# Optimization experiments

Hardware: AMD Instinct MI355X
Metric: run time of the kernel (lower is better)

## Reference

```python
import jax, jax.numpy as jnp
import numpy as np

N, E, G = 10000, 160000, 64
NODE_DIM, HID = 128, 256


def _edge_conv(x, src, dst, w1, b1, w2, b2):
    # gather endpoints: x_i = target features, x_j = source features (PyG source_to_target)
    x_i = x[dst]                              # [E, C]
    x_j = x[src]                              # [E, C]
    m = jnp.concatenate([x_i, x_j - x_i], axis=-1)  # [E, 2C]
    m = jax.nn.relu(m @ w1 + b1) @ w2 + b2          # [E, H]
    out = jax.ops.segment_max(m, dst, num_segments=N)  # scatter-max per target node
    return out  # nodes with no in-edges get -inf; subsequent relu maps them to 0 (matches PyG fill 0 + relu)


def setup_inputs() -> dict:
    key = jax.random.key(0)
    ks = jax.random.split(key, 20)
    x = jax.random.normal(ks[0], (N, NODE_DIM), dtype=jnp.float32)
    edge_index = jax.random.randint(ks[1], (2, E), 0, N)
    batch = jnp.sort(jax.random.randint(ks[2], (N,), 0, G))
    s = 0.05
    inp = {"x": x, "edge_index": edge_index, "batch": batch}
    dims = [(2 * NODE_DIM, HID), (2 * HID, HID), (2 * HID, HID)]
    for li, (din, dout) in enumerate(dims):
        inp[f"c{li}_w1"] = jax.random.normal(ks[3 + 4 * li], (din, dout), jnp.float32) * s
        inp[f"c{li}_b1"] = jnp.zeros((dout,), jnp.float32)
        inp[f"c{li}_w2"] = jax.random.normal(ks[4 + 4 * li], (dout, dout), jnp.float32) * s
        inp[f"c{li}_b2"] = jnp.zeros((dout,), jnp.float32)
    inp["cl_w1"] = jax.random.normal(ks[15], (2 * HID, HID), jnp.float32) * s
    inp["cl_b1"] = jnp.zeros((HID,), jnp.float32)
    inp["cl_w2"] = jax.random.normal(ks[16], (HID, 64), jnp.float32) * s
    inp["cl_b2"] = jnp.zeros((64,), jnp.float32)
    inp["cl_w3"] = jax.random.normal(ks[17], (64, 1), jnp.float32) * s
    inp["cl_b3"] = jnp.zeros((1,), jnp.float32)
    return inp


def reference(x, edge_index, batch,
              c0_w1, c0_b1, c0_w2, c0_b2,
              c1_w1, c1_b1, c1_w2, c1_b2,
              c2_w1, c2_b1, c2_w2, c2_b2,
              cl_w1, cl_b1, cl_w2, cl_b2, cl_w3, cl_b3):
    src, dst = edge_index[0], edge_index[1]
    for (w1, b1, w2, b2) in [(c0_w1, c0_b1, c0_w2, c0_b2),
                             (c1_w1, c1_b1, c1_w2, c1_b2),
                             (c2_w1, c2_b1, c2_w2, c2_b2)]:
        x = jax.nn.relu(_edge_conv(x, src, dst, w1, b1, w2, b2))
    # global mean / max pool per graph
    sums = jax.ops.segment_sum(x, batch, num_segments=G)
    counts = jax.ops.segment_sum(jnp.ones((x.shape[0], 1), x.dtype), batch, num_segments=G)
    x_mean = sums / jnp.maximum(counts, 1.0)
    x_max = jax.ops.segment_max(x, batch, num_segments=G)
    x_max = jnp.where(counts > 0, x_max, 0.0)
    h = jnp.concatenate([x_mean, x_max], axis=1)  # [G, 2H]
    h = jax.nn.relu(h @ cl_w1 + cl_b1)            # dropout is eval-mode identity
    h = jax.nn.relu(h @ cl_w2 + cl_b2)
    out = (h @ cl_w3 + cl_b3).squeeze(-1)         # [G]
    return out
```

## Files before the change

### kernel.cpp

```cpp
#include <hip/hip_runtime.h>


#define NN 10000
#define NE 160000
#define NG 64
#define NP 10048
#define EB 64

typedef __attribute__((ext_vector_type(8))) _Float16 f16x8;
typedef __attribute__((ext_vector_type(4))) _Float16 f16x4;
typedef __attribute__((ext_vector_type(4))) float f32x4;

__global__ void hist_kernel(const int* __restrict__ dstI, int* __restrict__ hist) {
    int i = blockIdx.x * blockDim.x + threadIdx.x;
    if (i < NE) atomicAdd(&hist[dstI[i]], 1);
}

__global__ void scan_kernel(const int* __restrict__ hist, int* __restrict__ cursor) {
    __shared__ int sums[256];
    const int t = threadIdx.x;
    const int per = (NN + 255) / 256;
    const int lo = t * per, hi = (lo + per < NN) ? lo + per : NN;
    int s = 0;
    for (int i = lo; i < hi; ++i) s += hist[i];
    sums[t] = s;
    __syncthreads();
    for (int ofs = 1; ofs < 256; ofs <<= 1) {
        int add = (t >= ofs) ? sums[t - ofs] : 0;
        __syncthreads();
        sums[t] += add;
        __syncthreads();
    }
    int run = sums[t] - s;
    for (int i = lo; i < hi; ++i) {
        int h = hist[i];
        cursor[i] = run;
        run += h;
    }
}

__global__ void scatter_kernel(const int* __restrict__ srcI, const int* __restrict__ dstI,
                               int* __restrict__ cursor,
                               int* __restrict__ se2, int* __restrict__ de2) {
    int i = blockIdx.x * blockDim.x + threadIdx.x;
    if (i < NE) {
        int d = dstI[i];
        int p = atomicAdd(&cursor[d], 1);
        se2[p] = srcI[i];
        de2[p] = d;
    }
}

__global__ void prep_weights(const float* __restrict__ w1, const float* __restrict__ w2, int C,
                             _Float16* __restrict__ WcT, _Float16* __restrict__ w2T) {
    int total1 = 512 * C;
    int total = total1 + 256 * 256;
    for (int i = blockIdx.x * blockDim.x + threadIdx.x; i < total; i += gridDim.x * blockDim.x) {
        if (i < total1) {
            int n = i / C, k = i - n * C;
            float v = (n < 256) ? (w1[k * 256 + n] - w1[(C + k) * 256 + n])
                                : w1[(C + k) * 256 + (n - 256)];
            WcT[n * C + k] = (_Float16)v;
        } else {
            int j = i - total1;
            int n = j >> 8, k = j & 255;
            w2T[n * 256 + k] = (_Float16)w2[k * 256 + n];
        }
    }
}

template <int C>
__global__ void conv_rows(const float* __restrict__ src, _Float16* __restrict__ xh) {
    const int total4 = NP * C / 4;
    const int c4 = C / 4;
    for (int i4 = blockIdx.x * blockDim.x + threadIdx.x; i4 < total4; i4 += gridDim.x * blockDim.x) {
        const int row = i4 / c4;
        f16x4 o;
        if (row < NN) {
            float4 v = ((const float4*)src)[i4];
            o[0] = (_Float16)v.x; o[1] = (_Float16)v.y;
            o[2] = (_Float16)v.z; o[3] = (_Float16)v.w;
        } else {
            o[0] = o[1] = o[2] = o[3] = (_Float16)0.f;
        }
        ((f16x4*)xh)[i4] = o;
    }
}

template <int C>
__global__ __launch_bounds__(256) void node_gemm(
    const _Float16* __restrict__ xh, const _Float16* __restrict__ WT,
    const float* __restrict__ b1, float* __restrict__ Af, _Float16* __restrict__ Bh) {
    const int wave = threadIdx.x >> 6, lane = threadIdx.x & 63;
    const int lrow = lane & 15, lk = (lane >> 4) * 8;
    const int r0 = blockIdx.x * 64;
    const int c0 = blockIdx.y * 256 + wave * 64;

    f32x4 acc[4][4] = {};
#pragma unroll
    for (int kk = 0; kk < C; kk += 32) {
        f16x8 ah[4];
#pragma unroll
        for (int m = 0; m < 4; ++m)
            ah[m] = *(const f16x8*)(xh + (size_t)(r0 + m * 16 + lrow) * C + kk + lk);
#pragma unroll
        for (int t = 0; t < 4; ++t) {
            f16x8 bh = *(const f16x8*)(WT + (size_t)(c0 + t * 16 + lrow) * C + kk + lk);
#pragma unroll
            for (int m = 0; m < 4; ++m)
                acc[m][t] = __builtin_amdgcn_mfma_f32_16x16x32_f16(ah[m], bh, acc[m][t], 0, 0, 0);
        }
    }
    if (blockIdx.y == 0) {
#pragma unroll
        for (int t = 0; t < 4; ++t) {
            const int col = c0 + t * 16 + lrow;
            const float bias = b1[col];
#pragma unroll
            for (int m = 0; m < 4; ++m)
#pragma unroll
                for (int j = 0; j < 4; ++j) {
                    const int row = r0 + m * 16 + (lane >> 4) * 4 + j;
                    Af[(size_t)row * 256 + col] = acc[m][t][j] + bias;
                }
        }
    } else {
#pragma unroll
        for (int t = 0; t < 4; ++t) {
            const int col = c0 - 256 + t * 16 + lrow;
#pragma unroll
            for (int m = 0; m < 4; ++m)
#pragma unroll
                for (int j = 0; j < 4; ++j) {
                    const int row = r0 + m * 16 + (lane >> 4) * 4 + j;
                    Bh[(size_t)row * 256 + col] = (_Float16)acc[m][t][j];
                }
        }
    }
}

__global__ __launch_bounds__(512, 4) void edge_gemm(
    const float* __restrict__ Af, const _Float16* __restrict__ Bh,
    const int* __restrict__ se2, const int* __restrict__ de2,
    const _Float16* __restrict__ w2T,
    const float* __restrict__ b2, float* __restrict__ y) {
    __shared__ _Float16 hh[EB * 256];
    const int tid = threadIdx.x;
    const int wave = tid >> 6, lane = tid & 63;

    const int orig = blockIdx.x;
    const int xcd = orig & 7, pos = orig >> 3;
    const int q = 2500 >> 3, r = 2500 & 7;
    const int bid = (xcd < r ? xcd * (q + 1) : r * (q + 1) + (xcd - r) * q) + pos;
    const int e0 = bid * EB;

    {
        int se[8], de[8];
#pragma unroll
        for (int i = 0; i < 8; ++i) {
            se[i] = se2[e0 + wave * 8 + i];
            de[i] = de2[e0 + wave * 8 + i];
        }
        float4 av[8];
        f16x4 bv[8];
#pragma unroll
        for (int i = 0; i < 8; ++i) {
            bv[i] = *(const f16x4*)(Bh + (size_t)se[i] * 256 + lane * 4);
            av[i] = *(const float4*)(Af + (size_t)de[i] * 256 + lane * 4);
        }
#pragma unroll
        for (int i = 0; i < 8; ++i) {
            const int el = wave * 8 + i;
            const int row = ((el >> 2) & 3) * 16 + (el >> 4) * 4 + (el & 3);
            f16x4 vh;
            vh[0] = (_Float16)fmaxf(av[i].x + (float)bv[i][0], 0.f);
            vh[1] = (_Float16)fmaxf(av[i].y + (float)bv[i][1], 0.f);
            vh[2] = (_Float16)fmaxf(av[i].z + (float)bv[i][2], 0.f);
            vh[3] = (_Float16)fmaxf(av[i].w + (float)bv[i][3], 0.f);
            const int idx = (row * 256 + lane * 4) ^ ((row & 7) << 3);
            *(f16x4*)(&hh[idx]) = vh;
        }
    }
    __syncthreads();

    const int lrow = lane & 15, lk = (lane >> 4) * 8;
    const _Float16* wbase = w2T + (size_t)(wave * 32 + lrow) * 256 + lk;

    f32x4 acc[4][2] = {};
    f16x8 bhA[2], bhB[2];
    bhA[0] = *(const f16x8*)(wbase);
    bhA[1] = *(const f16x8*)(wbase + 16 * 256);
#pragma unroll
    for (int kk = 0; kk < 256; kk += 32) {
        if (kk + 32 < 256) {
            bhB[0] = *(const f16x8*)(wbase + kk + 32);
            bhB[1] = *(const f16x8*)(wbase + 16 * 256 + kk + 32);
        }
        f16x8 ah[4];
#pragma unroll
        for (int m = 0; m < 4; ++m) {
            const int row = m * 16 + lrow;
            const int idx = (row * 256 + kk + lk) ^ ((row & 7) << 3);
            ah[m] = *(const f16x8*)(&hh[idx]);
        }
#pragma unroll
        for (int t = 0; t < 2; ++t)
#pragma unroll
            for (int m = 0; m < 4; ++m)
                acc[m][t] = __builtin_amdgcn_mfma_f32_16x16x32_f16(ah[m], bhA[t], acc[m][t], 0, 0, 0);
        bhA[0] = bhB[0];
        bhA[1] = bhB[1];
    }

    const int g = lane >> 4;
    int d[16];
#pragma unroll
    for (int k = 0; k < 16; ++k) d[k] = de2[e0 + g * 16 + k];
#pragma unroll
    for (int t = 0; t < 2; ++t) {
        const int col = wave * 32 + t * 16 + lrow;
        const float bias = b2[col];
        float run = acc[0][t][0];
        int dp = d[0];
#pragma unroll
        for (int k = 1; k < 16; ++k) {
            const float v = acc[k >> 2][t][k & 3];
            if (d[k] == dp) {
                run = fmaxf(run, v);
            } else {
                const float o = run + bias;
                if (o > 0.f) atomicMax((int*)(y + (size_t)dp * 256 + col), __float_as_int(o));
                run = v;
                dp = d[k];
            }
        }
        const float o = run + bias;
        if (o > 0.f) atomicMax((int*)(y + (size_t)dp * 256 + col), __float_as_int(o));
    }
}

__global__ void pool_kernel(const float* __restrict__ y, const int* __restrict__ batch,
                            float* __restrict__ pooled) {
    const int g = blockIdx.x;
    __shared__ int slo, shi;
    if (threadIdx.x == 0) {
        int lo = 0, hi = NN;
        while (lo < hi) { int m = (lo + hi) >> 1; if (batch[m] < g) lo = m + 1; else hi = m; }
        slo = lo;
        int lo2 = lo, hi2 = NN;
        while (lo2 < hi2) { int m = (lo2 + hi2) >> 1; if (batch[m] < g + 1) lo2 = m + 1; else hi2 = m; }
        shi = lo2;
    }
    __syncthreads();
    const int lo = slo, hi = shi, c = threadIdx.x;
    float s0 = 0.f, s1 = 0.f, s2 = 0.f, s3 = 0.f;
    float m0 = 0.f, m1 = 0.f, m2 = 0.f, m3 = 0.f;
    int n = lo;
    for (; n + 4 <= hi; n += 4) {
        float v0 = y[(size_t)(n + 0) * 256 + c];
        float v1 = y[(size_t)(n + 1) * 256 + c];
        float v2 = y[(size_t)(n + 2) * 256 + c];
        float v3 = y[(size_t)(n + 3) * 256 + c];
        s0 += v0; s1 += v1; s2 += v2; s3 += v3;
        m0 = fmaxf(m0, v0); m1 = fmaxf(m1, v1); m2 = fmaxf(m2, v2); m3 = fmaxf(m3, v3);
    }
    for (; n < hi; ++n) {
        float v = y[(size_t)n * 256 + c];
        s0 += v; m0 = fmaxf(m0, v);
    }
    const float s = (s0 + s1) + (s2 + s3);
    const float mx = fmaxf(fmaxf(m0, m1), fmaxf(m2, m3));
    const int cnt = hi - lo;
    pooled[g * 512 + c] = cnt ? s / (float)cnt : 0.f;
    pooled[g * 512 + 256 + c] = cnt ? mx : 0.f;
}

__global__ void classifier(const float* __restrict__ pooled,
                           const float* __restrict__ w1, const float* __restrict__ b1,
                           const float* __restrict__ w2, const float* __restrict__ b2,
                           const float* __restrict__ w3, const float* __restrict__ b3,
                           float* __restrict__ out) {
    const int g = blockIdx.x;
    __shared__ float ph[512];
    __shared__ float o1[256];
    __shared__ float o2[64];
    const int t = threadIdx.x;
    ph[t] = pooled[g * 512 + t];
    ph[t + 256] = pooled[g * 512 + 256 + t];
    __syncthreads();
    float s = 0.f;
    for (int k = 0; k < 512; ++k) s += ph[k] * w1[k * 256 + t];
    o1[t] = fmaxf(s + b1[t], 0.f);
    __syncthreads();
    if (t < 64) {
        float s2 = 0.f;
        for (int k = 0; k < 256; ++k) s2 += o1[k] * w2[k * 64 + t];
        o2[t] = fmaxf(s2 + b2[t], 0.f);
    }
    __syncthreads();
    if (t < 64) {
        float v = o2[t] * w3[t];
        for (int off = 32; off; off >>= 1) v += __shfl_down(v, off);
        if (t == 0) out[g] = v + b3[0];
    }
}

extern "C" void kernel_launch(void* const* d_in, const int* in_sizes, int n_in,
                              void* d_out, int out_size, void* d_ws, size_t ws_size,
                              hipStream_t stream) {
    (void)in_sizes; (void)n_in; (void)out_size; (void)ws_size;
    const float* x0 = (const float*)d_in[0];
    const int* eidx = (const int*)d_in[1];
    const int* batch = (const int*)d_in[2];
    const int* srcI = eidx;
    const int* dstI = eidx + NE;

    char* ws = (char*)d_ws;
    size_t off = 0;
    auto alloc = [&](size_t bytes) -> void* {
        void* p = ws + off;
        off += (bytes + 255) & ~(size_t)255;
        return p;
    };
    _Float16* xh = (_Float16*)alloc((size_t)NP * 256 * 2);
    float* Af = (float*)alloc((size_t)NP * 256 * 4);
    _Float16* Bh = (_Float16*)alloc((size_t)NP * 256 * 2);
    float* y  = (float*)alloc((size_t)NP * 256 * 4);
    _Float16* WcT = (_Float16*)alloc(512 * 256 * 2);
    _Float16* w2T = (_Float16*)alloc(256 * 256 * 2);
    float* pooled = (float*)alloc(64 * 512 * 4);
    int* hist = (int*)alloc(NN * 4);
    int* se2 = (int*)alloc(NE * 4);
    int* de2 = (int*)alloc(NE * 4);

    const float* lw[3][4] = {
        {(const float*)d_in[3],  (const float*)d_in[4],  (const float*)d_in[5],  (const float*)d_in[6]},
        {(const float*)d_in[7],  (const float*)d_in[8],  (const float*)d_in[9],  (const float*)d_in[10]},
        {(const float*)d_in[11], (const float*)d_in[12], (const float*)d_in[13], (const float*)d_in[14]},
    };

    hipMemsetAsync(hist, 0, NN * 4, stream);
    hist_kernel<<<dim3((NE + 255) / 256), dim3(256), 0, stream>>>(dstI, hist);
    scan_kernel<<<dim3(1), dim3(256), 0, stream>>>(hist, hist);
    scatter_kernel<<<dim3((NE + 255) / 256), dim3(256), 0, stream>>>(srcI, dstI, hist, se2, de2);

    conv_rows<128><<<dim3(1024), dim3(256), 0, stream>>>(x0, xh);

    for (int l = 0; l < 3; ++l) {
        const int C = (l == 0) ? 128 : 256;
        prep_weights<<<dim3(256), dim3(256), 0, stream>>>(lw[l][0], lw[l][2], C, WcT, w2T);
        if (C == 128)
            node_gemm<128><<<dim3(NP / 64, 2), dim3(256), 0, stream>>>(xh, WcT, lw[l][1], Af, Bh);
        else
            node_gemm<256><<<dim3(NP / 64, 2), dim3(256), 0, stream>>>(xh, WcT, lw[l][1], Af, Bh);
        hipMemsetAsync(y, 0, (size_t)NP * 256 * 4, stream);
        edge_gemm<<<dim3(NE / EB), dim3(512), 0, stream>>>(Af, Bh, se2, de2, w2T, lw[l][3], y);
        if (l < 2)
            conv_rows<256><<<dim3(1024), dim3(256), 0, stream>>>(y, xh);
    }

    pool_kernel<<<dim3(NG), dim3(256), 0, stream>>>(y, batch, pooled);
    classifier<<<dim3(NG), dim3(256), 0, stream>>>(pooled,
        (const float*)d_in[15], (const float*)d_in[16],
        (const float*)d_in[17], (const float*)d_in[18],
        (const float*)d_in[19], (const float*)d_in[20], (float*)d_out);
}
```

Before: 363.2 us.

## Fuse fp32-to-fp16 row conversion into node GEMM and preload edge weights

```diff
diff --git a/kernel.cpp b/kernel.cpp
--- a/kernel.cpp
+++ b/kernel.cpp
@@ -70,26 +70,8 @@
 }
 
 template <int C>
-__global__ void conv_rows(const float* __restrict__ src, _Float16* __restrict__ xh) {
-    const int total4 = NP * C / 4;
-    const int c4 = C / 4;
-    for (int i4 = blockIdx.x * blockDim.x + threadIdx.x; i4 < total4; i4 += gridDim.x * blockDim.x) {
-        const int row = i4 / c4;
-        f16x4 o;
-        if (row < NN) {
-            float4 v = ((const float4*)src)[i4];
-            o[0] = (_Float16)v.x; o[1] = (_Float16)v.y;
-            o[2] = (_Float16)v.z; o[3] = (_Float16)v.w;
-        } else {
-            o[0] = o[1] = o[2] = o[3] = (_Float16)0.f;
-        }
-        ((f16x4*)xh)[i4] = o;
-    }
-}
-
-template <int C>
 __global__ __launch_bounds__(256) void node_gemm(
-    const _Float16* __restrict__ xh, const _Float16* __restrict__ WT,
+    const float* __restrict__ xf, const _Float16* __restrict__ WT,
     const float* __restrict__ b1, float* __restrict__ Af, _Float16* __restrict__ Bh) {
     const int wave = threadIdx.x >> 6, lane = threadIdx.x & 63;
     const int lrow = lane & 15, lk = (lane >> 4) * 8;
@@ -101,8 +83,19 @@
     for (int kk = 0; kk < C; kk += 32) {
         f16x8 ah[4];
 #pragma unroll
-        for (int m = 0; m < 4; ++m)
-            ah[m] = *(const f16x8*)(xh + (size_t)(r0 + m * 16 + lrow) * C + kk + lk);
+        for (int m = 0; m < 4; ++m) {
+            int rc = r0 + m * 16 + lrow;
+            if (rc > NN - 1) rc = NN - 1;
+            const float* xp = xf + (size_t)rc * C + kk + lk;
+            const float4 v0 = *(const float4*)(xp);
+            const float4 v1 = *(const float4*)(xp + 4);
+            f16x8 a;
+            a[0] = (_Float16)v0.x; a[1] = (_Float16)v0.y;
+            a[2] = (_Float16)v0.z; a[3] = (_Float16)v0.w;
+            a[4] = (_Float16)v1.x; a[5] = (_Float16)v1.y;
+            a[6] = (_Float16)v1.z; a[7] = (_Float16)v1.w;
+            ah[m] = a;
+        }
 #pragma unroll
         for (int t = 0; t < 4; ++t) {
             f16x8 bh = *(const f16x8*)(WT + (size_t)(c0 + t * 16 + lrow) * C + kk + lk);
@@ -150,9 +143,14 @@
 
     const int orig = blockIdx.x;
     const int xcd = orig & 7, pos = orig >> 3;
-    const int q = 2500 >> 3, r = 2500 & 7;
-    const int bid = (xcd < r ? xcd * (q + 1) : r * (q + 1) + (xcd - r) * q) + pos;
+    const int qq = 2500 >> 3, rr = 2500 & 7;
+    const int bid = (xcd < rr ? xcd * (qq + 1) : rr * (qq + 1) + (xcd - rr) * qq) + pos;
     const int e0 = bid * EB;
+
+    const int lrow = lane & 15, lk = (lane >> 4) * 8;
+    const _Float16* wbase = w2T + (size_t)(wave * 32 + lrow) * 256 + lk;
+
+    f16x8 w0[8], w1[8];
 
     {
         int se[8], de[8];
@@ -167,6 +165,11 @@
         for (int i = 0; i < 8; ++i) {
             bv[i] = *(const f16x4*)(Bh + (size_t)se[i] * 256 + lane * 4);
             av[i] = *(const float4*)(Af + (size_t)de[i] * 256 + lane * 4);
+        }
+#pragma unroll
+        for (int q = 0; q < 4; ++q) {
+            w0[q]     = *(const f16x8*)(wbase + q * 32);
+            w0[4 + q] = *(const f16x8*)(wbase + 16 * 256 + q * 32);
         }
 #pragma unroll
         for (int i = 0; i < 8; ++i) {
@@ -183,19 +186,16 @@
     }
     __syncthreads();
 
-    const int lrow = lane & 15, lk = (lane >> 4) * 8;
-    const _Float16* wbase = w2T + (size_t)(wave * 32 + lrow) * 256 + lk;
+#pragma unroll
+    for (int q = 0; q < 4; ++q) {
+        w1[q]     = *(const f16x8*)(wbase + 128 + q * 32);
+        w1[4 + q] = *(const f16x8*)(wbase + 16 * 256 + 128 + q * 32);
+    }
 
     f32x4 acc[4][2] = {};
-    f16x8 bhA[2], bhB[2];
-    bhA[0] = *(const f16x8*)(wbase);
-    bhA[1] = *(const f16x8*)(wbase + 16 * 256);
-#pragma unroll
-    for (int kk = 0; kk < 256; kk += 32) {
-        if (kk + 32 < 256) {
-            bhB[0] = *(const f16x8*)(wbase + kk + 32);
-            bhB[1] = *(const f16x8*)(wbase + 16 * 256 + kk + 32);
-        }
+#pragma unroll
+    for (int q = 0; q < 4; ++q) {
+        const int kk = q * 32;
         f16x8 ah[4];
 #pragma unroll
         for (int m = 0; m < 4; ++m) {
@@ -204,12 +204,26 @@
             ah[m] = *(const f16x8*)(&hh[idx]);
         }
 #pragma unroll
-        for (int t = 0; t < 2; ++t)
-#pragma unroll
-            for (int m = 0; m < 4; ++m)
-                acc[m][t] = __builtin_amdgcn_mfma_f32_16x16x32_f16(ah[m], bhA[t], acc[m][t], 0, 0, 0);
-        bhA[0] = bhB[0];
-        bhA[1] = bhB[1];
+        for (int m = 0; m < 4; ++m) {
+            acc[m][0] = __builtin_amdgcn_mfma_f32_16x16x32_f16(ah[m], w0[q],     acc[m][0], 0, 0, 0);
+            acc[m][1] = __builtin_amdgcn_mfma_f32_16x16x32_f16(ah[m], w0[4 + q], acc[m][1], 0, 0, 0);
+        }
+    }
+#pragma unroll
+    for (int q = 0; q < 4; ++q) {
+        const int kk = 128 + q * 32;
+        f16x8 ah[4];
+#pragma unroll
+        for (int m = 0; m < 4; ++m) {
+            const int row = m * 16 + lrow;
+            const int idx = (row * 256 + kk + lk) ^ ((row & 7) << 3);
+            ah[m] = *(const f16x8*)(&hh[idx]);
+        }
+#pragma unroll
+        for (int m = 0; m < 4; ++m) {
+            acc[m][0] = __builtin_amdgcn_mfma_f32_16x16x32_f16(ah[m], w1[q],     acc[m][0], 0, 0, 0);
+            acc[m][1] = __builtin_amdgcn_mfma_f32_16x16x32_f16(ah[m], w1[4 + q], acc[m][1], 0, 0, 0);
+        }
     }
 
     const int g = lane >> 4;
@@ -322,7 +336,6 @@
         off += (bytes + 255) & ~(size_t)255;
         return p;
     };
-    _Float16* xh = (_Float16*)alloc((size_t)NP * 256 * 2);
     float* Af = (float*)alloc((size_t)NP * 256 * 4);
     _Float16* Bh = (_Float16*)alloc((size_t)NP * 256 * 2);
     float* y  = (float*)alloc((size_t)NP * 256 * 4);
@@ -344,19 +357,15 @@
     scan_kernel<<<dim3(1), dim3(256), 0, stream>>>(hist, hist);
     scatter_kernel<<<dim3((NE + 255) / 256), dim3(256), 0, stream>>>(srcI, dstI, hist, se2, de2);
 
-    conv_rows<128><<<dim3(1024), dim3(256), 0, stream>>>(x0, xh);
-
     for (int l = 0; l < 3; ++l) {
         const int C = (l == 0) ? 128 : 256;
         prep_weights<<<dim3(256), dim3(256), 0, stream>>>(lw[l][0], lw[l][2], C, WcT, w2T);
         if (C == 128)
-            node_gemm<128><<<dim3(NP / 64, 2), dim3(256), 0, stream>>>(xh, WcT, lw[l][1], Af, Bh);
+            node_gemm<128><<<dim3(NP / 64, 2), dim3(256), 0, stream>>>(x0, WcT, lw[l][1], Af, Bh);
         else
-            node_gemm<256><<<dim3(NP / 64, 2), dim3(256), 0, stream>>>(xh, WcT, lw[l][1], Af, Bh);
+            node_gemm<256><<<dim3(NP / 64, 2), dim3(256), 0, stream>>>(y, WcT, lw[l][1], Af, Bh);
         hipMemsetAsync(y, 0, (size_t)NP * 256 * 4, stream);
         edge_gemm<<<dim3(NE / EB), dim3(512), 0, stream>>>(Af, Bh, se2, de2, w2T, lw[l][3], y);
-        if (l < 2)
-            conv_rows<256><<<dim3(1024), dim3(256), 0, stream>>>(y, xh);
     }
 
     pool_kernel<<<dim3(NG), dim3(256), 0, stream>>>(y, batch, pooled);
```

Result: no change. 365.3 us (+0.6%).
